# Performance work log

Measured on AMD Instinct MI355X. Metric: run time of the kernel, lower is better.

## Reference

```python
import jax, jax.numpy as jnp
import numpy as np
from jax.scipy.special import logsumexp

T, B, D, L = 1024, 32, 768, 48
NEG = jnp.float32(-1e20)


def setup_inputs() -> dict:
    key = jax.random.key(0)
    ks = jax.random.split(key, 10)
    feats = jax.random.normal(ks[0], (T, B, D), jnp.float32)
    # tags: True = label disallowed at this position (partial annotation mask)
    tags = jax.random.uniform(ks[1], (T, B, L)) < 0.3
    lens = jax.random.randint(ks[2], (B,), T // 2, T + 1)
    W = jax.random.normal(ks[3], (D, L), jnp.float32) * 0.02
    b = jnp.zeros((L,), jnp.float32)
    base = jnp.float32(1.0 / L)
    begin_transition = jnp.full((L,), base) + 0.01 * jax.random.normal(ks[4], (L,), jnp.float32)
    transitions = jnp.full((L, L), base) + 0.01 * jax.random.normal(ks[5], (L, L), jnp.float32)
    end_transition = jnp.full((L,), base) + 0.01 * jax.random.normal(ks[6], (L,), jnp.float32)
    begin_constraints = jax.random.uniform(ks[7], (L,)) < 0.2
    end_constraints = jax.random.uniform(ks[8], (L,)) < 0.2
    transition_constraints = jax.random.uniform(ks[9], (L, L)) < 0.2
    return {
        "feats": feats, "tags": tags, "lens": lens,
        "W": W, "b": b,
        "begin_transition": begin_transition, "transitions": transitions,
        "end_transition": end_transition,
        "begin_constraints": begin_constraints, "end_constraints": end_constraints,
        "transition_constraints": transition_constraints,
    }


def _crf_logZ(emissions, begin, trans, end, tag_mask, lens):
    """Forward algorithm over [T,B,L] emissions; tag_mask True = disallowed.
    Returns log partition per batch element, read out at step lens-1."""
    fs0 = emissions[0] + begin[None, :]              # [B, L]
    fs0 = jnp.where(tag_mask[0], NEG, fs0)

    def step(prev, xs):
        em_t, m_t = xs
        # new[b, j] = logsumexp_k(prev[b, k] + trans[j, k]) + em_t[b, j]
        new = logsumexp(prev[:, None, :] + trans[None, :, :], axis=-1) + em_t
        new = jnp.where(m_t, NEG, new)
        return new, new

    _, ys = jax.lax.scan(step, fs0, (emissions[1:], tag_mask[1:]))
    all_fs = jnp.concatenate([fs0[None], ys], axis=0)        # [T, B, L]
    last = all_fs[lens - 1, jnp.arange(lens.shape[0])]       # [B, L]
    return logsumexp(last + end[None, :], axis=-1)           # [B]


def reference(feats, tags, lens, W, b, begin_transition, transitions,
              end_transition, begin_constraints, end_constraints,
              transition_constraints):
    # feature2labels (Dropout is identity in eval)
    emissions = jnp.einsum('tbd,dl->tbl', feats, W) + b      # [T, B, L]
    no_mask = jnp.zeros_like(tags)

    # forward_alg: unconstrained partition function
    fwd = _crf_logZ(emissions, begin_transition, transitions,
                    end_transition, no_mask, lens)

    # partial_score: constrained params + gold tag masking
    begin_m = jnp.where(begin_constraints, NEG, begin_transition)
    trans_m = jnp.where(transition_constraints, NEG, transitions)
    end_m = jnp.where(end_constraints, NEG, end_transition)
    par = _crf_logZ(emissions, begin_m, trans_m, end_m, tags, lens)

    # criterion per batch element (sum over batch = original scalar loss)
    return fwd - par                                          # [B]
```

## Files before the change

### kernel.cpp

```cpp
#include <hip/hip_runtime.h>

#define T_ 1024
#define B_ 32
#define D_ 768
#define L_ 48
#define TB_ (T_ * B_)

typedef __attribute__((ext_vector_type(4))) float f32x4;

__global__ __launch_bounds__(256, 2) void emis_gemm(
    const float* __restrict__ feats, const float* __restrict__ W,
    const float* __restrict__ bias, float* __restrict__ E) {
  __shared__ float fbuf[64 * 64];
  __shared__ float wbuf[48 * 68];
  const int tid = threadIdx.x;
  const int wv = tid >> 6;
  const int lane = tid & 63;
  const int cg = tid & 7;
  const int rg = tid >> 3;
  const int c0 = cg * 6;
  const int rowbase = blockIdx.x * 64;
  const int r7 = rg & 7;
  const int r_in = lane >> 4;
  const int slot = lane & 15;

  float acc[2][6];
#pragma unroll
  for (int i = 0; i < 2; i++)
#pragma unroll
    for (int c = 0; c < 6; c++) acc[i][c] = 0.f;

  for (int kc = 0; kc < D_; kc += 64) {
    __syncthreads();

#pragma unroll
    for (int inst = 0; inst < 4; inst++) {
      const int rowstart = wv * 16 + inst * 4;
      const int r = rowstart + r_in;
      const int gch = slot ^ (r & 7);
      const float* g = feats + (size_t)(rowbase + r) * D_ + kc + gch * 4;
      float* l = fbuf + rowstart * 64;
      __builtin_amdgcn_global_load_lds(
          (const __attribute__((address_space(1))) uint32_t*)g,
          (__attribute__((address_space(3))) uint32_t*)l, 16, 0, 0);
    }

#pragma unroll
    for (int i = 0; i < 12; i++) {
      const int idx = tid + i * 256;
      const int ko = idx / 48;
      const int j = idx - ko * 48;
      wbuf[j * 68 + ko] = W[(kc + ko) * L_ + j];
    }

    __syncthreads();

#pragma unroll 4
    for (int k4 = 0; k4 < 16; k4++) {
      float4 fv[2];
      float4 wv4[6];
      const int sch = (k4 ^ r7) << 2;
#pragma unroll
      for (int i = 0; i < 2; i++)
        fv[i] = *(const float4*)(fbuf + (rg + 32 * i) * 64 + sch);
#pragma unroll
      for (int cc = 0; cc < 6; cc++)
        wv4[cc] = *(const float4*)(wbuf + (c0 + cc) * 68 + k4 * 4);
#pragma unroll
      for (int i = 0; i < 2; i++) {
#pragma unroll
        for (int cc = 0; cc < 6; cc++) {
          acc[i][cc] = fmaf(fv[i].x, wv4[cc].x, acc[i][cc]);
          acc[i][cc] = fmaf(fv[i].y, wv4[cc].y, acc[i][cc]);
          acc[i][cc] = fmaf(fv[i].z, wv4[cc].z, acc[i][cc]);
          acc[i][cc] = fmaf(fv[i].w, wv4[cc].w, acc[i][cc]);
        }
      }
    }
  }

#pragma unroll
  for (int i = 0; i < 2; i++) {
    float* dst = E + (size_t)(rowbase + rg + 32 * i) * L_ + c0;
#pragma unroll
    for (int cc = 0; cc < 6; cc += 2) {
      float2 v;
      v.x = __expf(acc[i][cc + 0] + bias[c0 + cc + 0]);
      v.y = __expf(acc[i][cc + 1] + bias[c0 + cc + 1]);
      *(float2*)(dst + cc) = v;
    }
  }
}

__global__ __launch_bounds__(64)
__attribute__((amdgpu_waves_per_eu(1))) void crf_scan(
    const float* __restrict__ E, const int* __restrict__ tags,
    const int* __restrict__ lens, const float* __restrict__ begin,
    const float* __restrict__ trans, const float* __restrict__ endt,
    const int* __restrict__ bc, const int* __restrict__ ec,
    const int* __restrict__ tc, float* __restrict__ out) {
  __shared__ __align__(16) float sbuf[2][64];
  const int s = blockIdx.x;
  const int pass = s & 1;
  const int b = s >> 1;
  const int lane = threadIdx.x;
  const bool act = lane < L_;
  const bool par = (pass == 1);
  const int len = lens[b];
  const int stride = B_ * L_;
  const int base = b * L_ + (act ? lane : 0);

  float P[L_];
#pragma unroll
  for (int k = 0; k < L_; k++) P[k] = 0.f;
  if (act) {
#pragma unroll
    for (int k = 0; k < L_; k++) {
      float v = __expf(trans[lane * L_ + k]);
      if (par && tc[lane * L_ + k]) v = 0.f;
      P[k] = v;
    }
  }

  float a = 0.f;
  if (act) {
    a = E[base] * __expf(begin[lane]);
    if (par && (bc[lane] || tags[base])) a = 0.f;
  }
  float logacc = 0.f;

  sbuf[0][lane] = a;

  auto step = [&](int i, float ev, int tg, bool resc) {
    const f32x4* src = (const f32x4*)sbuf[i & 1];
    float s0 = 0.f, s1 = 0.f, s2 = 0.f, s3 = 0.f;
    f32x4 mx = {0.f, 0.f, 0.f, 0.f};
#pragma unroll
    for (int c = 0; c < 12; c++) {
      const f32x4 q = src[c];
      if (resc) {
        mx.x = fmaxf(mx.x, q.x);
        mx.y = fmaxf(mx.y, q.y);
        mx.z = fmaxf(mx.z, q.z);
        mx.w = fmaxf(mx.w, q.w);
      }
      s0 = fmaf(q.x, P[4 * c + 0], s0);
      s1 = fmaf(q.y, P[4 * c + 1], s1);
      s2 = fmaf(q.z, P[4 * c + 2], s2);
      s3 = fmaf(q.w, P[4 * c + 3], s3);
    }
    float evp = ev;
    if (resc) {
      float m = fmaxf(fmaxf(mx.x, mx.y), fmaxf(mx.z, mx.w));
      m = fmaxf(m, 1e-30f);
      logacc += __logf(m);
      evp = ev * (1.f / m);
    }
    float u = ((s0 + s1) + (s2 + s3)) * evp;
    if (tg) u = 0.f;
    a = u;
    sbuf[(i + 1) & 1][lane] = u;
  };

  float e4[4];
  int tg4[4];
#pragma unroll
  for (int i = 0; i < 4; i++) {
    e4[i] = E[(size_t)(1 + i) * stride + base];
    tg4[i] = par ? tags[(size_t)(1 + i) * stride + base] : 0;
  }

  int t = 1;
  for (; t + 4 <= len; t += 4) {
    float p4[4];
    int q4[4];
#pragma unroll
    for (int i = 0; i < 4; i++) {
      int tt = t + 4 + i;
      tt = (tt < len) ? tt : (len - 1);
      p4[i] = E[(size_t)tt * stride + base];
      q4[i] = par ? tags[(size_t)tt * stride + base] : 0;
    }
    if ((t & 7) == 1) {
      step(0, e4[0], tg4[0], true);
    } else {
      step(0, e4[0], tg4[0], false);
    }
    step(1, e4[1], tg4[1], false);
    step(2, e4[2], tg4[2], false);
    step(3, e4[3], tg4[3], false);
#pragma unroll
    for (int i = 0; i < 4; i++) { e4[i] = p4[i]; tg4[i] = q4[i]; }
  }
#pragma unroll
  for (int i = 0; i < 4; i++) {
    if (t + i < len) step(i, e4[i], tg4[i], false);
  }

  float z = 0.f;
  if (act) {
    float ez = __expf(endt[lane]);
    if (par && ec[lane]) ez = 0.f;
    z = a * ez;
  }
#pragma unroll
  for (int off = 32; off; off >>= 1) z += __shfl_xor(z, off, 64);
  const float logZ = logacc + __logf(z);
  if (lane == 0) atomicAdd(out + b, par ? -logZ : logZ);
}

extern "C" void kernel_launch(void* const* d_in, const int* in_sizes, int n_in,
                              void* d_out, int out_size, void* d_ws,
                              size_t ws_size, hipStream_t stream) {
  (void)in_sizes; (void)n_in; (void)out_size; (void)ws_size;
  const float* feats = (const float*)d_in[0];
  const int* tags = (const int*)d_in[1];
  const int* lens = (const int*)d_in[2];
  const float* W = (const float*)d_in[3];
  const float* bias = (const float*)d_in[4];
  const float* begin = (const float*)d_in[5];
  const float* trans = (const float*)d_in[6];
  const float* endt = (const float*)d_in[7];
  const int* bc = (const int*)d_in[8];
  const int* ec = (const int*)d_in[9];
  const int* tc = (const int*)d_in[10];

  float* E = (float*)d_ws;
  float* out = (float*)d_out;

  hipMemsetAsync(d_out, 0, B_ * sizeof(float), stream);

  emis_gemm<<<dim3(TB_ / 64), dim3(256), 0, stream>>>(feats, W, bias, E);
  crf_scan<<<dim3(2 * B_), dim3(64), 0, stream>>>(E, tags, lens, begin, trans,
                                                  endt, bc, ec, tc, out);
}
```

Before: 425.7 us.

## Rework GEMM tiling and cut CRF scan register footprint with LDS-held transitions

The emission GEMM now uses 128 threads, each computing 4 rows instead of 2. It replaces the async global-to-LDS loads and XOR swizzle with plain float4 loads into a padded LDS tile. The CRF scan keeps only 32 of the 48 transition columns in registers and reads the remaining 16 from LDS through a volatile pointer. It also drops the waves_per_eu(1) attribute and shortens the time-loop unroll and prefetch depth from 4 to 2. These changes aim to reduce register pressure and change occupancy, but they add LDS reads to the serial recurrence and lose the asynchronous load path in the GEMM.

```diff
diff --git a/kernel.cpp b/kernel.cpp
--- a/kernel.cpp
+++ b/kernel.cpp
@@ -8,25 +8,20 @@
 
 typedef __attribute__((ext_vector_type(4))) float f32x4;
 
-__global__ __launch_bounds__(256, 2) void emis_gemm(
+__global__ __launch_bounds__(128) void emis_gemm(
     const float* __restrict__ feats, const float* __restrict__ W,
     const float* __restrict__ bias, float* __restrict__ E) {
-  __shared__ float fbuf[64 * 64];
+  __shared__ float fbuf[64 * 68];
   __shared__ float wbuf[48 * 68];
   const int tid = threadIdx.x;
-  const int wv = tid >> 6;
-  const int lane = tid & 63;
   const int cg = tid & 7;
   const int rg = tid >> 3;
   const int c0 = cg * 6;
   const int rowbase = blockIdx.x * 64;
-  const int r7 = rg & 7;
-  const int r_in = lane >> 4;
-  const int slot = lane & 15;
-
-  float acc[2][6];
-#pragma unroll
-  for (int i = 0; i < 2; i++)
+
+  float acc[4][6];
+#pragma unroll
+  for (int i = 0; i < 4; i++)
 #pragma unroll
     for (int c = 0; c < 6; c++) acc[i][c] = 0.f;
 
@@ -34,20 +29,18 @@
     __syncthreads();
 
 #pragma unroll
-    for (int inst = 0; inst < 4; inst++) {
-      const int rowstart = wv * 16 + inst * 4;
-      const int r = rowstart + r_in;
-      const int gch = slot ^ (r & 7);
-      const float* g = feats + (size_t)(rowbase + r) * D_ + kc + gch * 4;
-      float* l = fbuf + rowstart * 64;
-      __builtin_amdgcn_global_load_lds(
-          (const __attribute__((address_space(1))) uint32_t*)g,
-          (__attribute__((address_space(3))) uint32_t*)l, 16, 0, 0);
-    }
-
-#pragma unroll
-    for (int i = 0; i < 12; i++) {
-      const int idx = tid + i * 256;
+    for (int i = 0; i < 8; i++) {
+      const int idx = tid + i * 128;
+      const int r = idx >> 4;
+      const int ch = idx & 15;
+      const float4 v =
+          *(const float4*)(feats + (size_t)(rowbase + r) * D_ + kc + ch * 4);
+      *(float4*)(fbuf + r * 68 + ch * 4) = v;
+    }
+
+#pragma unroll
+    for (int i = 0; i < 24; i++) {
+      const int idx = tid + i * 128;
       const int ko = idx / 48;
       const int j = idx - ko * 48;
       wbuf[j * 68 + ko] = W[(kc + ko) * L_ + j];
@@ -57,17 +50,16 @@
 
 #pragma unroll 4
     for (int k4 = 0; k4 < 16; k4++) {
-      float4 fv[2];
+      float4 fv[4];
       float4 wv4[6];
-      const int sch = (k4 ^ r7) << 2;
-#pragma unroll
-      for (int i = 0; i < 2; i++)
-        fv[i] = *(const float4*)(fbuf + (rg + 32 * i) * 64 + sch);
+#pragma unroll
+      for (int i = 0; i < 4; i++)
+        fv[i] = *(const float4*)(fbuf + (rg + 16 * i) * 68 + k4 * 4);
 #pragma unroll
       for (int cc = 0; cc < 6; cc++)
         wv4[cc] = *(const float4*)(wbuf + (c0 + cc) * 68 + k4 * 4);
 #pragma unroll
-      for (int i = 0; i < 2; i++) {
+      for (int i = 0; i < 4; i++) {
 #pragma unroll
         for (int cc = 0; cc < 6; cc++) {
           acc[i][cc] = fmaf(fv[i].x, wv4[cc].x, acc[i][cc]);
@@ -80,8 +72,8 @@
   }
 
 #pragma unroll
-  for (int i = 0; i < 2; i++) {
-    float* dst = E + (size_t)(rowbase + rg + 32 * i) * L_ + c0;
+  for (int i = 0; i < 4; i++) {
+    float* dst = E + (size_t)(rowbase + rg + 16 * i) * L_ + c0;
 #pragma unroll
     for (int cc = 0; cc < 6; cc += 2) {
       float2 v;
@@ -92,14 +84,14 @@
   }
 }
 
-__global__ __launch_bounds__(64)
-__attribute__((amdgpu_waves_per_eu(1))) void crf_scan(
+__global__ __launch_bounds__(64) void crf_scan(
     const float* __restrict__ E, const int* __restrict__ tags,
     const int* __restrict__ lens, const float* __restrict__ begin,
     const float* __restrict__ trans, const float* __restrict__ endt,
     const int* __restrict__ bc, const int* __restrict__ ec,
     const int* __restrict__ tc, float* __restrict__ out) {
   __shared__ __align__(16) float sbuf[2][64];
+  __shared__ float pbuf[16][64];
   const int s = blockIdx.x;
   const int pass = s & 1;
   const int b = s >> 1;
@@ -110,17 +102,26 @@
   const int stride = B_ * L_;
   const int base = b * L_ + (act ? lane : 0);
 
-  float P[L_];
-#pragma unroll
-  for (int k = 0; k < L_; k++) P[k] = 0.f;
-  if (act) {
-#pragma unroll
-    for (int k = 0; k < L_; k++) {
-      float v = __expf(trans[lane * L_ + k]);
+  float Pr[32];
+#pragma unroll
+  for (int k = 0; k < 32; k++) {
+    float v = 0.f;
+    if (act) {
+      v = __expf(trans[lane * L_ + k]);
       if (par && tc[lane * L_ + k]) v = 0.f;
-      P[k] = v;
-    }
-  }
+    }
+    Pr[k] = v;
+  }
+#pragma unroll
+  for (int kk = 0; kk < 16; kk++) {
+    float v = 0.f;
+    if (act) {
+      v = __expf(trans[lane * L_ + 32 + kk]);
+      if (par && tc[lane * L_ + 32 + kk]) v = 0.f;
+    }
+    pbuf[kk][lane] = v;
+  }
+  volatile const float* pv = &pbuf[0][0];
 
   float a = 0.f;
   if (act) {
@@ -131,12 +132,12 @@
 
   sbuf[0][lane] = a;
 
-  auto step = [&](int i, float ev, int tg, bool resc) {
-    const f32x4* src = (const f32x4*)sbuf[i & 1];
+  auto step = [&](int par_in, float ev, int tg, bool resc) {
+    const f32x4* src = (const f32x4*)sbuf[par_in];
     float s0 = 0.f, s1 = 0.f, s2 = 0.f, s3 = 0.f;
     f32x4 mx = {0.f, 0.f, 0.f, 0.f};
 #pragma unroll
-    for (int c = 0; c < 12; c++) {
+    for (int c = 0; c < 8; c++) {
       const f32x4 q = src[c];
       if (resc) {
         mx.x = fmaxf(mx.x, q.x);
@@ -144,10 +145,25 @@
         mx.z = fmaxf(mx.z, q.z);
         mx.w = fmaxf(mx.w, q.w);
       }
-      s0 = fmaf(q.x, P[4 * c + 0], s0);
-      s1 = fmaf(q.y, P[4 * c + 1], s1);
-      s2 = fmaf(q.z, P[4 * c + 2], s2);
-      s3 = fmaf(q.w, P[4 * c + 3], s3);
+      s0 = fmaf(q.x, Pr[4 * c + 0], s0);
+      s1 = fmaf(q.y, Pr[4 * c + 1], s1);
+      s2 = fmaf(q.z, Pr[4 * c + 2], s2);
+      s3 = fmaf(q.w, Pr[4 * c + 3], s3);
+    }
+#pragma unroll
+    for (int c = 8; c < 12; c++) {
+      const f32x4 q = src[c];
+      if (resc) {
+        mx.x = fmaxf(mx.x, q.x);
+        mx.y = fmaxf(mx.y, q.y);
+        mx.z = fmaxf(mx.z, q.z);
+        mx.w = fmaxf(mx.w, q.w);
+      }
+      const int kk = 4 * (c - 8);
+      s0 = fmaf(q.x, pv[(kk + 0) * 64 + lane], s0);
+      s1 = fmaf(q.y, pv[(kk + 1) * 64 + lane], s1);
+      s2 = fmaf(q.z, pv[(kk + 2) * 64 + lane], s2);
+      s3 = fmaf(q.w, pv[(kk + 3) * 64 + lane], s3);
     }
     float evp = ev;
     if (resc) {
@@ -159,43 +175,38 @@
     float u = ((s0 + s1) + (s2 + s3)) * evp;
     if (tg) u = 0.f;
     a = u;
-    sbuf[(i + 1) & 1][lane] = u;
+    sbuf[par_in ^ 1][lane] = u;
   };
 
-  float e4[4];
-  int tg4[4];
-#pragma unroll
-  for (int i = 0; i < 4; i++) {
-    e4[i] = E[(size_t)(1 + i) * stride + base];
-    tg4[i] = par ? tags[(size_t)(1 + i) * stride + base] : 0;
+  float e2[2];
+  int tg2[2];
+#pragma unroll
+  for (int i = 0; i < 2; i++) {
+    e2[i] = E[(size_t)(1 + i) * stride + base];
+    tg2[i] = par ? tags[(size_t)(1 + i) * stride + base] : 0;
   }
 
   int t = 1;
-  for (; t + 4 <= len; t += 4) {
-    float p4[4];
-    int q4[4];
-#pragma unroll
-    for (int i = 0; i < 4; i++) {
-      int tt = t + 4 + i;
+  for (; t + 2 <= len; t += 2) {
+    float p2[2];
+    int q2[2];
+#pragma unroll
+    for (int i = 0; i < 2; i++) {
+      int tt = t + 2 + i;
       tt = (tt < len) ? tt : (len - 1);
-      p4[i] = E[(size_t)tt * stride + base];
-      q4[i] = par ? tags[(size_t)tt * stride + base] : 0;
+      p2[i] = E[(size_t)tt * stride + base];
+      q2[i] = par ? tags[(size_t)tt * stride + base] : 0;
     }
     if ((t & 7) == 1) {
-      step(0, e4[0], tg4[0], true);
+      step(0, e2[0], tg2[0], true);
     } else {
-      step(0, e4[0], tg4[0], false);
-    }
-    step(1, e4[1], tg4[1], false);
-    step(2, e4[2], tg4[2], false);
-    step(3, e4[3], tg4[3], false);
-#pragma unroll
-    for (int i = 0; i < 4; i++) { e4[i] = p4[i]; tg4[i] = q4[i]; }
-  }
-#pragma unroll
-  for (int i = 0; i < 4; i++) {
-    if (t + i < len) step(i, e4[i], tg4[i], false);
-  }
+      step(0, e2[0], tg2[0], false);
+    }
+    step(1, e2[1], tg2[1], false);
+    e2[0] = p2[0]; e2[1] = p2[1];
+    tg2[0] = q2[0]; tg2[1] = q2[1];
+  }
+  if (t < len) step(0, e2[0], tg2[0], false);
 
   float z = 0.f;
   if (act) {
@@ -230,7 +241,7 @@
 
   hipMemsetAsync(d_out, 0, B_ * sizeof(float), stream);
 
-  emis_gemm<<<dim3(TB_ / 64), dim3(256), 0, stream>>>(feats, W, bias, E);
+  emis_gemm<<<dim3(TB_ / 64), dim3(128), 0, stream>>>(feats, W, bias, E);
   crf_scan<<<dim3(2 * B_), dim3(64), 0, stream>>>(E, tags, lens, begin, trans,
                                                   endt, bc, ec, tc, out);
 }
```

Result: slower. 958.7 us (+125.2%).
